# Performance work log

Hardware: AMD Instinct MI355X
Metric: run time of the kernel (lower is better)

The kernel has to match this reference:

```python
import jax, jax.numpy as jnp
import numpy as np

EPS = 1e-5
LOSS_WEIGHT = 0.3
IGNORE_INDEX = -100


def rmsnorm(x, w):
    # x: (B,S,D), w: (D,)
    var = jnp.mean(x * x, axis=-1, keepdims=True)
    return x * jax.lax.rsqrt(var + EPS) * w


def cross_entropy(logits, targets):
    # logits: (B,T,V), targets: (B,T) int; ignore_index=-100, mean reduction
    logp = jax.nn.log_softmax(logits, axis=-1)
    valid = targets != IGNORE_INDEX
    safe_t = jnp.where(valid, targets, 0)
    nll = -jnp.take_along_axis(logp, safe_t[..., None], axis=-1)[..., 0]
    nll = jnp.where(valid, nll, 0.0)
    return jnp.sum(nll) / jnp.maximum(jnp.sum(valid), 1)


def setup_inputs() -> dict:
    key = jax.random.key(0)
    ks = jax.random.split(key, 5)
    B, S, D, V, H = 1, 2048, 1024, 50257, 3
    hidden = jax.random.normal(ks[0], (B, S, D), dtype=jnp.float32)
    targets = jax.random.randint(ks[1], (B, S), 0, V, dtype=jnp.int64)
    emb_w = jax.random.normal(ks[2], (V, D), dtype=jnp.float32) * 0.02
    main_norm_w = jnp.ones((D,), dtype=jnp.float32)
    aux_proj_w = jax.random.normal(ks[3], (H - 1, D, D), dtype=jnp.float32) * 0.02
    aux_norm_w = jnp.ones((H - 1, D), dtype=jnp.float32)
    aux_out_w = jax.random.normal(ks[4], (H - 1, V, D), dtype=jnp.float32) * 0.02
    return {"hidden": hidden, "targets": targets, "emb_w": emb_w,
            "main_norm_w": main_norm_w, "aux_proj_w": aux_proj_w,
            "aux_norm_w": aux_norm_w, "aux_out_w": aux_out_w}


def reference(hidden, targets, emb_w, main_norm_w, aux_proj_w, aux_norm_w, aux_out_w):
    # Main head: norm -> tied vocab projection
    main_logits = jnp.einsum('bsd,vd->bsv', rmsnorm(hidden, main_norm_w), emb_w)
    main_loss = cross_entropy(main_logits[:, :-1, :], targets[:, 1:])

    # Auxiliary heads predict t+2, t+3, ...
    n_aux = aux_proj_w.shape[0]
    aux_losses = []
    for i in range(n_aux):
        k = i + 2
        h = jnp.einsum('bsd,ed->bse', hidden, aux_proj_w[i])  # d_model -> d_model
        logits = jnp.einsum('bsd,vd->bsv', rmsnorm(h, aux_norm_w[i]), aux_out_w[i])
        aux_losses.append(cross_entropy(logits[:, :-k, :], targets[:, k:]))
    total_aux = sum(aux_losses) / len(aux_losses) if aux_losses else jnp.float32(0.0)
    loss = main_loss + LOSS_WEIGHT * total_aux
    return main_logits, loss
```

## Files before the change

kernel.cpp:

```cpp
#include <hip/hip_runtime.h>
#include <hip/hip_bf16.h>


typedef __hip_bfloat16 bf16;
typedef __attribute__((ext_vector_type(8))) short bf16x8;
typedef __attribute__((ext_vector_type(4))) float f32x4;

typedef const __attribute__((address_space(1))) void* gptr_t;
typedef __attribute__((address_space(3))) void* lptr_t;

#define S_LEN   2048
#define DMODEL  1024
#define VOCAB   50257
#define VPAD2   51200
#define NT128   400

__device__ __forceinline__ void gload_lds16(const void* g, void* l) {
  __builtin_amdgcn_global_load_lds((gptr_t)g, (lptr_t)l, 16, 0, 0);
}

__global__ __launch_bounds__(256) void k_cvt(const float* __restrict__ src,
                                             bf16* __restrict__ dst,
                                             long rows_src, long rows_pad) {
  const long total4 = rows_pad << 8;
  for (long i = (long)blockIdx.x * 256 + threadIdx.x; i < total4;
       i += (long)gridDim.x * 256) {
    const long e = i << 2;
    const long row = e >> 10;
    alignas(8) bf16 o[4];
    if (row < rows_src) {
      const float4 v = *(const float4*)(src + e);
      o[0] = __float2bfloat16(v.x); o[1] = __float2bfloat16(v.y);
      o[2] = __float2bfloat16(v.z); o[3] = __float2bfloat16(v.w);
    } else {
      o[0] = o[1] = o[2] = o[3] = __float2bfloat16(0.f);
    }
    *(uint2*)(dst + e) = *(const uint2*)o;
  }
}

__global__ __launch_bounds__(256) void k_rms(const float* __restrict__ x,
                                             const float* __restrict__ w,
                                             bf16* __restrict__ xn) {
  const int row = blockIdx.x;
  const int t = threadIdx.x;
  const float4 v = ((const float4*)(x + (size_t)row * DMODEL))[t];
  float ss = v.x*v.x + v.y*v.y + v.z*v.z + v.w*v.w;
  #pragma unroll
  for (int d = 1; d < 64; d <<= 1) ss += __shfl_xor(ss, d, 64);
  __shared__ float red[4];
  if ((t & 63) == 0) red[t >> 6] = ss;
  __syncthreads();
  const float tot = red[0] + red[1] + red[2] + red[3];
  const float scale = rsqrtf(tot * (1.f / DMODEL) + 1e-5f);
  const float4 wv = ((const float4*)w)[t];
  alignas(8) bf16 o[4];
  o[0] = __float2bfloat16(v.x * scale * wv.x);
  o[1] = __float2bfloat16(v.y * scale * wv.y);
  o[2] = __float2bfloat16(v.z * scale * wv.z);
  o[3] = __float2bfloat16(v.w * scale * wv.w);
  *(uint2*)(xn + (size_t)row * DMODEL + t * 4) = *(const uint2*)o;
}

template<bool WRITE_OUT>
__global__ __launch_bounds__(256, 2)
void k_gemm128(const bf16* __restrict__ A, const bf16* __restrict__ B,
               float* __restrict__ C, long ldc, int Nvalid,
               const int* __restrict__ targets, int shift,
               float* __restrict__ pmax, float* __restrict__ psum,
               float* __restrict__ ptgt, int ntiles) {
  constexpr int K = DMODEL;
  __shared__ bf16 As[128 * 32];
  __shared__ bf16 Bs[128 * 32];
  __shared__ float lds_m[128][2];
  __shared__ float lds_s[128][2];
  __shared__ int lds_tgt[128];

  const int t = threadIdx.x;
  const int w = t >> 6, l = t & 63, g = l >> 4, q = l & 15;
  const int wr = w >> 1, wc = w & 1;
  const int id = blockIdx.x;
  const int bm = (id >> 3) & 15;
  const int bn = (id & 7) * 50 + (id >> 7);

  f32x4 acc[4][4];
  #pragma unroll
  for (int i = 0; i < 4; ++i)
    #pragma unroll
    for (int j = 0; j < 4; ++j)
      #pragma unroll
      for (int r = 0; r < 4; ++r) acc[i][j][r] = 0.f;

  char* lA0 = (char*)As + w * 1024;
  char* lA1 = (char*)As + 4096 + w * 1024;
  char* lB0 = (char*)Bs + w * 1024;
  char* lB1 = (char*)Bs + 4096 + w * 1024;
  const int scol = ((t & 3) * 16) ^ (((t >> 5) & 1) * 32);
  const char* gA0 = (const char*)(A + (size_t)(bm * 128 + (t >> 2)) * K) + scol;
  const char* gA1 = gA0 + (size_t)64 * K * 2;
  const char* gB0 = (const char*)(B + (size_t)(bn * 128 + (t >> 2)) * K) + scol;
  const char* gB1 = gB0 + (size_t)64 * K * 2;

  const int laneoff = (q * 64 + g * 16) ^ (((q >> 3) & 1) << 5);
  const char* rdA = (const char*)As + wr * 4096 + laneoff;
  const char* rdB = (const char*)Bs + wc * 4096 + laneoff;

  for (int k0 = 0; k0 < K; k0 += 32) {
    const int kb = k0 * 2;
    gload_lds16(gA0 + kb, lA0);
    gload_lds16(gA1 + kb, lA1);
    gload_lds16(gB0 + kb, lB0);
    gload_lds16(gB1 + kb, lB1);
    __syncthreads();
    bf16x8 a[4], b[4];
    #pragma unroll
    for (int mi = 0; mi < 4; ++mi) a[mi] = *(const bf16x8*)(rdA + mi * 1024);
    #pragma unroll
    for (int ni = 0; ni < 4; ++ni) b[ni] = *(const bf16x8*)(rdB + ni * 1024);
    __builtin_amdgcn_s_setprio(1);
    #pragma unroll
    for (int mi = 0; mi < 4; ++mi)
      #pragma unroll
      for (int ni = 0; ni < 4; ++ni)
        acc[mi][ni] = __builtin_amdgcn_mfma_f32_16x16x32_bf16(a[mi], b[ni], acc[mi][ni], 0, 0, 0);
    __builtin_amdgcn_s_setprio(0);
    __syncthreads();
  }

  if constexpr (WRITE_OUT) {
    #pragma unroll
    for (int mi = 0; mi < 4; ++mi) {
      #pragma unroll
      for (int r = 0; r < 4; ++r) {
        const long row = bm * 128 + wr * 64 + mi * 16 + g * 4 + r;
        #pragma unroll
        for (int ni = 0; ni < 4; ++ni) {
          const int col = bn * 128 + wc * 64 + ni * 16 + q;
          if (col < Nvalid) C[row * ldc + col] = acc[mi][ni][r];
        }
      }
    }
  }

  if (t < 128) {
    const int rowg = bm * 128 + t;
    lds_tgt[t] = (rowg < S_LEN - shift) ? targets[rowg + shift] : -1;
  }
  __syncthreads();
  #pragma unroll
  for (int mi = 0; mi < 4; ++mi) {
    #pragma unroll
    for (int r = 0; r < 4; ++r) {
      const int rl = wr * 64 + mi * 16 + g * 4 + r;
      const int tgt = lds_tgt[rl];
      float v[4];
      #pragma unroll
      for (int ni = 0; ni < 4; ++ni) {
        const int n = bn * 128 + wc * 64 + ni * 16 + q;
        const float av = acc[mi][ni][r];
        if (n == tgt) ptgt[bm * 128 + rl] = av;
        v[ni] = (n < Nvalid) ? av : -1e30f;
      }
      float m = fmaxf(fmaxf(v[0], v[1]), fmaxf(v[2], v[3]));
      #pragma unroll
      for (int d = 1; d < 16; d <<= 1) m = fmaxf(m, __shfl_xor(m, d, 64));
      float s = 0.f;
      #pragma unroll
      for (int ni = 0; ni < 4; ++ni) s += __expf(v[ni] - m);
      #pragma unroll
      for (int d = 1; d < 16; d <<= 1) s += __shfl_xor(s, d, 64);
      if (q == 0) { lds_m[rl][wc] = m; lds_s[rl][wc] = s; }
    }
  }
  __syncthreads();
  if (t < 128) {
    const float m0 = lds_m[t][0], m1 = lds_m[t][1];
    const float s0 = lds_s[t][0], s1 = lds_s[t][1];
    const float M = fmaxf(m0, m1);
    const float Ssum = s0 * __expf(m0 - M) + s1 * __expf(m1 - M);
    const size_t idx = (size_t)(bm * 128 + t) * ntiles + bn;
    pmax[idx] = M;
    psum[idx] = Ssum;
  }
}

__global__ __launch_bounds__(256, 2)
void k_gemm(const bf16* __restrict__ A, const bf16* __restrict__ B,
            float* __restrict__ C, long ldc, int Nvalid) {
  constexpr int K = DMODEL;
  __shared__ bf16 As[128 * 32];
  __shared__ bf16 Bs[128 * 32];

  const int t = threadIdx.x;
  const int bn = blockIdx.x, bm = blockIdx.y;
  const int w = t >> 6, l = t & 63, g = l >> 4, q = l & 15;
  const int wr = w >> 1, wc = w & 1;

  f32x4 acc[4][4];
  #pragma unroll
  for (int i = 0; i < 4; ++i)
    #pragma unroll
    for (int j = 0; j < 4; ++j)
      #pragma unroll
      for (int r = 0; r < 4; ++r) acc[i][j][r] = 0.f;

  char* lA0 = (char*)As + w * 1024;
  char* lA1 = (char*)As + 4096 + w * 1024;
  char* lB0 = (char*)Bs + w * 1024;
  char* lB1 = (char*)Bs + 4096 + w * 1024;
  const char* gA0 = (const char*)(A + (size_t)(bm * 128 + (t >> 2)) * K) + (t & 3) * 16;
  const char* gA1 = gA0 + (size_t)64 * K * 2;
  const char* gB0 = (const char*)(B + (size_t)(bn * 128 + (t >> 2)) * K) + (t & 3) * 16;
  const char* gB1 = gB0 + (size_t)64 * K * 2;

  for (int k0 = 0; k0 < K; k0 += 32) {
    const int kb = k0 * 2;
    gload_lds16(gA0 + kb, lA0);
    gload_lds16(gA1 + kb, lA1);
    gload_lds16(gB0 + kb, lB0);
    gload_lds16(gB1 + kb, lB1);
    __syncthreads();
    bf16x8 a[4], b[4];
    #pragma unroll
    for (int mi = 0; mi < 4; ++mi)
      a[mi] = *(const bf16x8*)&As[(wr * 64 + mi * 16 + q) * 32 + g * 8];
    #pragma unroll
    for (int ni = 0; ni < 4; ++ni)
      b[ni] = *(const bf16x8*)&Bs[(wc * 64 + ni * 16 + q) * 32 + g * 8];
    #pragma unroll
    for (int mi = 0; mi < 4; ++mi)
      #pragma unroll
      for (int ni = 0; ni < 4; ++ni)
        acc[mi][ni] = __builtin_amdgcn_mfma_f32_16x16x32_bf16(a[mi], b[ni], acc[mi][ni], 0, 0, 0);
    __syncthreads();
  }

  #pragma unroll
  for (int mi = 0; mi < 4; ++mi) {
    #pragma unroll
    for (int r = 0; r < 4; ++r) {
      const long row = bm * 128 + wr * 64 + mi * 16 + g * 4 + r;
      #pragma unroll
      for (int ni = 0; ni < 4; ++ni) {
        const int col = bn * 128 + wc * 64 + ni * 16 + q;
        if (col < Nvalid) C[row * ldc + col] = acc[mi][ni][r];
      }
    }
  }
}

__global__ __launch_bounds__(64) void k_combine(const float* __restrict__ pmax,
                                                const float* __restrict__ psum,
                                                const float* __restrict__ ptgt,
                                                float* __restrict__ nll,
                                                int ntiles, int nv) {
  const int r = blockIdx.x;
  const int l = threadIdx.x;
  float M = -1e30f, Ssum = 0.f;
  for (int tl = l; tl < ntiles; tl += 64) {
    const float m = pmax[(size_t)r * ntiles + tl];
    const float s = psum[(size_t)r * ntiles + tl];
    const float nM = fmaxf(M, m);
    Ssum = Ssum * __expf(M - nM) + s * __expf(m - nM);
    M = nM;
  }
  #pragma unroll
  for (int d = 1; d < 64; d <<= 1) {
    const float m2 = __shfl_xor(M, d, 64);
    const float s2 = __shfl_xor(Ssum, d, 64);
    const float nM = fmaxf(M, m2);
    Ssum = Ssum * __expf(M - nM) + s2 * __expf(m2 - nM);
    M = nM;
  }
  if (l == 0) nll[r] = (r < nv) ? (M + logf(Ssum) - ptgt[r]) : 0.f;
}

__global__ __launch_bounds__(256) void k_loss(const float* __restrict__ nll,
                                              float* __restrict__ out) {
  __shared__ float sh[256];
  const int t = threadIdx.x;
  float sums[3];
  #pragma unroll
  for (int h = 0; h < 3; ++h) {
    const int nv = 2047 - h;
    float s = 0.f;
    for (int r = t; r < nv; r += 256) s += nll[h * 2048 + r];
    sh[t] = s; __syncthreads();
    for (int off = 128; off > 0; off >>= 1) {
      if (t < off) sh[t] += sh[t + off];
      __syncthreads();
    }
    sums[h] = sh[0]; __syncthreads();
  }
  if (t == 0)
    out[0] = sums[0] / 2047.f + 0.3f * 0.5f * (sums[1] / 2046.f + sums[2] / 2045.f);
}

extern "C" void kernel_launch(void* const* d_in, const int* in_sizes, int n_in,
                              void* d_out, int out_size, void* d_ws, size_t ws_size,
                              hipStream_t stream) {
  const float* hidden      = (const float*)d_in[0];
  const int*   targets     = (const int*)d_in[1];
  const float* emb_w       = (const float*)d_in[2];
  const float* main_norm_w = (const float*)d_in[3];
  const float* aux_proj_w  = (const float*)d_in[4];
  const float* aux_norm_w  = (const float*)d_in[5];
  const float* aux_out_w   = (const float*)d_in[6];
  float* out = (float*)d_out;

  char* ws = (char*)d_ws;
  bf16*  Wb    = (bf16*)(ws);
  bf16*  hb    = (bf16*)(ws + 104857600);
  bf16*  xn    = (bf16*)(ws + 109051904);
  bf16*  projb = (bf16*)(ws + 113246208);
  float* hbuf  = (float*)(ws + 117440512);
  float* pmax  = (float*)(ws + 125829120);
  float* psum  = (float*)(ws + 129105920);
  float* ptgt  = (float*)(ws + 132382720);
  float* nll   = (float*)(ws + 132390912);

  k_cvt<<<2048, 256, 0, stream>>>(hidden, hb, 2048, 2048);
  k_cvt<<<2048, 256, 0, stream>>>(aux_proj_w, projb, 2048, 2048);
  k_rms<<<2048, 256, 0, stream>>>(hidden, main_norm_w, xn);

  k_cvt<<<2048, 256, 0, stream>>>(emb_w, Wb, VOCAB, VPAD2);
  k_gemm128<true><<<6400, 256, 0, stream>>>(
      xn, Wb, out, VOCAB, VOCAB, targets, 1, pmax, psum, ptgt, NT128);
  k_combine<<<2048, 64, 0, stream>>>(pmax, psum, ptgt, nll, NT128, 2047);

  for (int i = 0; i < 2; ++i) {
    k_cvt<<<2048, 256, 0, stream>>>(aux_out_w + (size_t)i * VOCAB * DMODEL, Wb, VOCAB, VPAD2);
    k_gemm<<<dim3(8, 16), 256, 0, stream>>>(
        hb, projb + (size_t)i * DMODEL * DMODEL, hbuf, DMODEL, DMODEL);
    k_rms<<<2048, 256, 0, stream>>>(hbuf, aux_norm_w + (size_t)i * DMODEL, xn);
    k_gemm128<false><<<6400, 256, 0, stream>>>(
        xn, Wb, nullptr, 0, VOCAB, targets, i + 2, pmax, psum, ptgt, NT128);
    k_combine<<<2048, 64, 0, stream>>>(pmax, psum, ptgt, nll + (i + 1) * 2048, NT128, 2048 - (i + 2));
  }

  k_loss<<<1, 256, 0, stream>>>(nll, out + (size_t)S_LEN * VOCAB);
}
```

Baseline: 1.146 ms.

## Cut vocab padding tiles, widen K-step to 64, and use nontemporal logit stores

Vocab padding shrinks from 51200 to 50304 rows, so each vocab GEMM launches 393 column tiles (6288 blocks) instead of 400, with the leftover tile handled by a separate block mapping. Each main-loop iteration now loads a 64-wide K slab into a doubled LDS buffer and runs two MFMA groups. That halves the number of barrier pairs and loop iterations, at the cost of twice the LDS. Logit writes use nontemporal stores to keep the large output from polluting the cache. The extra LDS may lower occupancy.

```diff
diff --git a/kernel.cpp b/kernel.cpp
--- a/kernel.cpp
+++ b/kernel.cpp
@@ -12,8 +12,9 @@
 #define S_LEN   2048
 #define DMODEL  1024
 #define VOCAB   50257
-#define VPAD2   51200
-#define NT128   400
+#define NPADR   50304
+#define NT128   393
+#define NBLK    6288
 
 __device__ __forceinline__ void gload_lds16(const void* g, void* l) {
   __builtin_amdgcn_global_load_lds((gptr_t)g, (lptr_t)l, 16, 0, 0);
@@ -69,9 +70,8 @@
                const int* __restrict__ targets, int shift,
                float* __restrict__ pmax, float* __restrict__ psum,
                float* __restrict__ ptgt, int ntiles) {
-  constexpr int K = DMODEL;
-  __shared__ bf16 As[128 * 32];
-  __shared__ bf16 Bs[128 * 32];
+  __shared__ bf16 As[2][128 * 32];
+  __shared__ bf16 Bs[2][128 * 32];
   __shared__ float lds_m[128][2];
   __shared__ float lds_s[128][2];
   __shared__ int lds_tgt[128];
@@ -80,8 +80,15 @@
   const int w = t >> 6, l = t & 63, g = l >> 4, q = l & 15;
   const int wr = w >> 1, wc = w & 1;
   const int id = blockIdx.x;
-  const int bm = (id >> 3) & 15;
-  const int bn = (id & 7) * 50 + (id >> 7);
+  int bm, bn;
+  if (id < 6272) {
+    const int x = id & 7, u = id >> 3;
+    bm = u & 15;
+    bn = x * 49 + (u >> 4);
+  } else {
+    bm = id - 6272;
+    bn = 392;
+  }
 
   f32x4 acc[4][4];
   #pragma unroll
@@ -91,32 +98,45 @@
       #pragma unroll
       for (int r = 0; r < 4; ++r) acc[i][j][r] = 0.f;
 
-  char* lA0 = (char*)As + w * 1024;
-  char* lA1 = (char*)As + 4096 + w * 1024;
-  char* lB0 = (char*)Bs + w * 1024;
-  char* lB1 = (char*)Bs + 4096 + w * 1024;
+  char* dA = (char*)As + w * 1024;
+  char* dB = (char*)Bs + w * 1024;
   const int scol = ((t & 3) * 16) ^ (((t >> 5) & 1) * 32);
-  const char* gA0 = (const char*)(A + (size_t)(bm * 128 + (t >> 2)) * K) + scol;
-  const char* gA1 = gA0 + (size_t)64 * K * 2;
-  const char* gB0 = (const char*)(B + (size_t)(bn * 128 + (t >> 2)) * K) + scol;
-  const char* gB1 = gB0 + (size_t)64 * K * 2;
+  const char* gA0 = (const char*)(A + (size_t)(bm * 128 + (t >> 2)) * DMODEL) + scol;
+  const char* gA1 = gA0 + (size_t)64 * DMODEL * 2;
+  const char* gB0 = (const char*)(B + (size_t)(bn * 128 + (t >> 2)) * DMODEL) + scol;
+  const char* gB1 = gB0 + (size_t)64 * DMODEL * 2;
 
   const int laneoff = (q * 64 + g * 16) ^ (((q >> 3) & 1) << 5);
   const char* rdA = (const char*)As + wr * 4096 + laneoff;
   const char* rdB = (const char*)Bs + wc * 4096 + laneoff;
 
-  for (int k0 = 0; k0 < K; k0 += 32) {
-    const int kb = k0 * 2;
-    gload_lds16(gA0 + kb, lA0);
-    gload_lds16(gA1 + kb, lA1);
-    gload_lds16(gB0 + kb, lB0);
-    gload_lds16(gB1 + kb, lB1);
+  for (int k0 = 0; k0 < 16; ++k0) {
+    const int kb = k0 * 128;
+    gload_lds16(gA0 + kb, dA);
+    gload_lds16(gA1 + kb, dA + 4096);
+    gload_lds16(gA0 + kb + 64, dA + 8192);
+    gload_lds16(gA1 + kb + 64, dA + 12288);
+    gload_lds16(gB0 + kb, dB);
+    gload_lds16(gB1 + kb, dB + 4096);
+    gload_lds16(gB0 + kb + 64, dB + 8192);
+    gload_lds16(gB1 + kb + 64, dB + 12288);
     __syncthreads();
     bf16x8 a[4], b[4];
     #pragma unroll
     for (int mi = 0; mi < 4; ++mi) a[mi] = *(const bf16x8*)(rdA + mi * 1024);
     #pragma unroll
     for (int ni = 0; ni < 4; ++ni) b[ni] = *(const bf16x8*)(rdB + ni * 1024);
+    __builtin_amdgcn_s_setprio(1);
+    #pragma unroll
+    for (int mi = 0; mi < 4; ++mi)
+      #pragma unroll
+      for (int ni = 0; ni < 4; ++ni)
+        acc[mi][ni] = __builtin_amdgcn_mfma_f32_16x16x32_bf16(a[mi], b[ni], acc[mi][ni], 0, 0, 0);
+    __builtin_amdgcn_s_setprio(0);
+    #pragma unroll
+    for (int mi = 0; mi < 4; ++mi) a[mi] = *(const bf16x8*)(rdA + 8192 + mi * 1024);
+    #pragma unroll
+    for (int ni = 0; ni < 4; ++ni) b[ni] = *(const bf16x8*)(rdB + 8192 + ni * 1024);
     __builtin_amdgcn_s_setprio(1);
     #pragma unroll
     for (int mi = 0; mi < 4; ++mi)
@@ -136,7 +156,8 @@
         #pragma unroll
         for (int ni = 0; ni < 4; ++ni) {
           const int col = bn * 128 + wc * 64 + ni * 16 + q;
-          if (col < Nvalid) C[row * ldc + col] = acc[mi][ni][r];
+          if (col < Nvalid)
+            __builtin_nontemporal_store(acc[mi][ni][r], &C[row * ldc + col]);
         }
       }
     }
@@ -323,17 +344,17 @@
   k_cvt<<<2048, 256, 0, stream>>>(aux_proj_w, projb, 2048, 2048);
   k_rms<<<2048, 256, 0, stream>>>(hidden, main_norm_w, xn);
 
-  k_cvt<<<2048, 256, 0, stream>>>(emb_w, Wb, VOCAB, VPAD2);
-  k_gemm128<true><<<6400, 256, 0, stream>>>(
+  k_cvt<<<2048, 256, 0, stream>>>(emb_w, Wb, VOCAB, NPADR);
+  k_gemm128<true><<<NBLK, 256, 0, stream>>>(
       xn, Wb, out, VOCAB, VOCAB, targets, 1, pmax, psum, ptgt, NT128);
   k_combine<<<2048, 64, 0, stream>>>(pmax, psum, ptgt, nll, NT128, 2047);
 
   for (int i = 0; i < 2; ++i) {
-    k_cvt<<<2048, 256, 0, stream>>>(aux_out_w + (size_t)i * VOCAB * DMODEL, Wb, VOCAB, VPAD2);
+    k_cvt<<<2048, 256, 0, stream>>>(aux_out_w + (size_t)i * VOCAB * DMODEL, Wb, VOCAB, NPADR);
     k_gemm<<<dim3(8, 16), 256, 0, stream>>>(
         hb, projb + (size_t)i * DMODEL * DMODEL, hbuf, DMODEL, DMODEL);
     k_rms<<<2048, 256, 0, stream>>>(hbuf, aux_norm_w + (size_t)i * DMODEL, xn);
-    k_gemm128<false><<<6400, 256, 0, stream>>>(
+    k_gemm128<false><<<NBLK, 256, 0, stream>>>(
         xn, Wb, nullptr, 0, VOCAB, targets, i + 2, pmax, psum, ptgt, NT128);
     k_combine<<<2048, 64, 0, stream>>>(pmax, psum, ptgt, nll + (i + 1) * 2048, NT128, 2048 - (i + 2));
   }
```

Measured after the change: 1.029 ms. 10.2% less time.
